# Kernel optimization log

Measured on AMD Instinct MI355X. Metric: run time of the kernel, lower is better.

The kernel has to match this reference:

```python
import jax, jax.numpy as jnp
import numpy as np

IN_MODES = (4, 4, 8, 8, 4)
OUT_MODES = (4, 4, 8, 8, 4)
RANKS = (1, 8, 8, 8, 8, 1)
N_TOKENS = 8192


def setup_inputs() -> dict:
    key = jax.random.key(0)
    ks = jax.random.split(key, 7)
    inp = jax.random.normal(ks[0], (N_TOKENS, int(np.prod(IN_MODES))), dtype=jnp.float32)
    cores = []
    for i in range(5):
        shape = (IN_MODES[i], RANKS[i], RANKS[i + 1], OUT_MODES[i])
        # kaiming-uniform-like small init to keep the 5-core chain numerically tame
        fan_in = shape[0] * shape[1] * shape[2]
        bound = float(np.sqrt(3.0 / fan_in))
        cores.append(jax.random.uniform(ks[i + 1], shape, minval=-bound, maxval=bound, dtype=jnp.float32))
    biases = jax.random.uniform(ks[6], (int(np.prod(OUT_MODES)),), minval=-0.05, maxval=0.05, dtype=jnp.float32)
    return {
        "input": inp,
        "core0": cores[0], "core1": cores[1], "core2": cores[2],
        "core3": cores[3], "core4": cores[4],
        "biases": biases,
    }


def reference(input, core0, core1, core2, core3, core4, biases):
    # reshape tokens into the 5 input modes: [N, a, b, c, d, e]
    x = input.reshape((-1,) + IN_MODES)
    # TT contraction. Original einsum has no '->'; free indices h (ranks[0]=1)
    # and m (ranks[5]=1) are size-1 boundary ranks, so summing them out here is
    # equivalent to the original reshape-squeeze.
    out = jnp.einsum(
        'nabcde,ahiv,bijw,cjkx,dkly,elmz->nvwxyz',
        x, core0, core1, core2, core3, core4,
        optimize='optimal',
    )
    out = out.reshape(-1, int(np.prod(OUT_MODES)))
    return out + biases
```

## Files before the change

kernel.cpp:

```cpp
#include <hip/hip_runtime.h>

#define DIM 4096

typedef __bf16 bf16x8 __attribute__((ext_vector_type(8)));
typedef float floatx4 __attribute__((ext_vector_type(4)));

__device__ __forceinline__ void async_ld16(void* lds, const void* g) {
  __builtin_amdgcn_global_load_lds(
      (const __attribute__((address_space(1))) unsigned int*)g,
      (__attribute__((address_space(3))) unsigned int*)lds, 16, 0, 0);
}

__global__ void build_k(const float* __restrict__ c0, const float* __restrict__ c1,
                        const float* __restrict__ c2, const float* __restrict__ c3,
                        const float* __restrict__ c4,
                        float* __restrict__ K012, float* __restrict__ K34T) {
  const int bid = blockIdx.x, tid = threadIdx.x;
  if (bid < 512) {
    __shared__ float K01s[128];
    const int abc = bid >> 2;
    const int ab = abc >> 3, c = abc & 7;
    if (tid < 128) {
      const int a = ab >> 2, b = ab & 3;
      const int j = tid >> 4, vw = tid & 15, v = vw >> 2, w = vw & 3;
      float s = 0.f;
#pragma unroll
      for (int i = 0; i < 8; ++i)
        s += c0[a * 32 + i * 4 + v] * c1[b * 256 + i * 32 + j * 4 + w];
      K01s[tid] = s;
    }
    __syncthreads();
    const int t = bid * 256 + tid;
    const int vwx = t & 127, k = (t >> 7) & 7;
    const int vw = vwx >> 3, xx = vwx & 7;
    float s = 0.f;
#pragma unroll
    for (int j = 0; j < 8; ++j)
      s += K01s[j * 16 + vw] * c2[c * 512 + j * 64 + k * 8 + xx];
    K012[t] = s;
  } else {
    const int u = (bid - 512) * 256 + tid;
    const int yz = u & 31, kk = (u >> 5) & 7, de = u >> 8;
    const int d = de >> 2, e = de & 3, y = yz >> 2, z = yz & 3;
    float s = 0.f;
#pragma unroll
    for (int l = 0; l < 8; ++l)
      s += c3[d * 512 + kk * 64 + l * 8 + y] * c4[e * 32 + l * 4 + z];
    K34T[kk * 1024 + yz * 32 + de] = s;
  }
}

__global__ void build_wt_conv(const float* __restrict__ K012, const float* __restrict__ K34T,
                              __bf16* __restrict__ WT,
                              const float* __restrict__ X, __bf16* __restrict__ Xb) {
  const int bid = blockIdx.x, tid = threadIdx.x;
  if (bid < 8192) {
    const long t = (long)bid * 256 + tid;
    const long e8 = t * 8;
    const int in = (int)(e8 & 4095), o = (int)(e8 >> 12);
    const int de0 = in & 31, abc = in >> 5;
    const int yz = o & 31, vwx = o >> 5;
    const float* kp = K012 + abc * 1024 + vwx;
    const float* vp = K34T + yz * 32 + de0;
    float s[8] = {};
#pragma unroll
    for (int k = 0; k < 8; ++k) {
      const float a = kp[k * 128];
      const float4 v0 = *(const float4*)(vp + k * 1024);
      const float4 v1 = *(const float4*)(vp + k * 1024 + 4);
      s[0] += a * v0.x; s[1] += a * v0.y; s[2] += a * v0.z; s[3] += a * v0.w;
      s[4] += a * v1.x; s[5] += a * v1.y; s[6] += a * v1.z; s[7] += a * v1.w;
    }
    bf16x8 w;
#pragma unroll
    for (int d = 0; d < 8; ++d) w[d] = (__bf16)s[d];
    ((bf16x8*)WT)[t] = w;
  } else {
    const long t = (long)(bid - 8192) * 256 + tid;
    const float4 a = ((const float4*)X)[t * 2];
    const float4 b = ((const float4*)X)[t * 2 + 1];
    bf16x8 w;
    w[0] = (__bf16)a.x; w[1] = (__bf16)a.y; w[2] = (__bf16)a.z; w[3] = (__bf16)a.w;
    w[4] = (__bf16)b.x; w[5] = (__bf16)b.y; w[6] = (__bf16)b.z; w[7] = (__bf16)b.w;
    ((bf16x8*)Xb)[t] = w;
  }
}


#define SB0()  __builtin_amdgcn_sched_barrier(0)
#define LGKM0() asm volatile("s_waitcnt lgkmcnt(0)" ::: "memory")
#define VM6()  asm volatile("s_waitcnt vmcnt(6)" ::: "memory")
#define BAR()  __builtin_amdgcn_s_barrier()
#define P1() __builtin_amdgcn_s_setprio(1)
#define P0() __builtin_amdgcn_s_setprio(0)

#define STA(p, h, koff) do { \
  async_ld16(&As[p][(h) * 128][0] + ldsq[0], agp[0] + (h) * 524288 + (koff)); \
  async_ld16(&As[p][(h) * 128][0] + ldsq[1], agp[1] + (h) * 524288 + (koff)); } while (0)
#define STB(p, h, koff) do { \
  async_ld16(&Bs[p][(h) * 128][0] + ldsq[0], bgp[0] + (h) * 524288 + (koff)); \
  async_ld16(&Bs[p][(h) * 128][0] + ldsq[1], bgp[1] + (h) * 524288 + (koff)); } while (0)

#define RDA(p, mh) do { \
  _Pragma("unroll") for (int fi = 0; fi < 4; ++fi) { \
    const int row = ((mh) * 8 + 2 * fi + wm) * 16 + lm; \
    _Pragma("unroll") for (int kh = 0; kh < 2; ++kh) \
      af[fi][kh] = *(const bf16x8*)&As[p][row][((kh * 4 + kq) ^ (row & 7)) * 8]; \
  } } while (0)
#define RDB(p, nh, sl) do { \
  _Pragma("unroll") for (int gi = 0; gi < 2; ++gi) { \
    const int row = (4 * ((nh) * 2 + gi) + wn) * 16 + lm; \
    _Pragma("unroll") for (int kh = 0; kh < 2; ++kh) \
      bs[sl][gi][kh] = *(const bf16x8*)&Bs[p][row][((kh * 4 + kq) ^ (row & 7)) * 8]; \
  } } while (0)

#define MMAQ(sl, mh, nh) do { \
  _Pragma("unroll") for (int fi = 0; fi < 4; ++fi) \
  _Pragma("unroll") for (int gi = 0; gi < 2; ++gi) \
  _Pragma("unroll") for (int kh = 0; kh < 2; ++kh) \
    acc[(mh) * 4 + fi][(nh) * 2 + gi] = __builtin_amdgcn_mfma_f32_16x16x32_bf16( \
        af[fi][kh], bs[sl][gi][kh], acc[(mh) * 4 + fi][(nh) * 2 + gi], 0, 0, 0); } while (0)

__global__ __launch_bounds__(512, 2) void gemm_8ph(const __bf16* __restrict__ A,
                                                   const __bf16* __restrict__ WT,
                                                   const float* __restrict__ bias,
                                                   float* __restrict__ C) {
  __shared__ __bf16 As[2][256][64];
  __shared__ __bf16 Bs[2][256][64];

  const int tid = threadIdx.x;
  const int gb = (blockIdx.x & 7) * 64 + (blockIdx.x >> 3);
  const int m0 = (gb >> 4) * 256;
  const int n0 = (gb & 15) * 256;

  const int wave = tid >> 6, lane = tid & 63;
  const int wm = wave & 1, wn = wave >> 1;
  const int lm = lane & 15, kq = lane >> 4;

  floatx4 acc[8][4] = {};
  bf16x8 af[4][2], bs[2][2][2];

  const __bf16* agp[2];
  const __bf16* bgp[2];
  int ldsq[2];
#pragma unroll
  for (int j = 0; j < 2; ++j) {
    const int q = tid + j * 512;
    const int r = q >> 3, pc = q & 7;
    const int c = pc ^ (r & 7);
    ldsq[j] = q * 8;
    agp[j] = A + (long)(m0 + r) * DIM + c * 8;
    bgp[j] = WT + (long)(n0 + r) * DIM + c * 8;
  }

  STB(0, 0, 0); STA(0, 0, 0); STB(0, 1, 0); STA(0, 1, 0); STB(1, 0, 64);
  STA(1, 0, 64); STB(1, 1, 64); STA(1, 1, 64);
  VM6();
  BAR(); SB0();
  RDB(0, 0, 0);

#pragma unroll 1
  for (int it = 0; it < 32; ++it) {
    int t2 = 2 * it + 2; if (t2 > 63) t2 = 63;
    int t3 = 2 * it + 3; if (t3 > 63) t3 = 63;
    const int k2 = t2 * 64, k3 = t3 * 64;

    RDA(0, 0); STB(0, 0, k2);
    BAR(); LGKM0(); SB0(); P1(); MMAQ(0, 0, 0); P0(); BAR(); SB0();

    RDB(0, 1, 1); STA(0, 0, k2);
    BAR(); LGKM0(); SB0(); P1(); MMAQ(1, 0, 1); P0(); BAR(); SB0();

    RDA(0, 1); STB(0, 1, k2);
    BAR(); LGKM0(); SB0(); P1(); MMAQ(1, 1, 1); P0(); BAR(); SB0();

    RDB(1, 0, 1); STA(0, 1, k2);
    BAR(); SB0(); P1(); MMAQ(0, 1, 0); P0();
    LGKM0();
    VM6();
    BAR(); SB0();

    RDA(1, 0); STB(1, 0, k3);
    BAR(); LGKM0(); SB0(); P1(); MMAQ(1, 0, 0); P0(); BAR(); SB0();

    RDB(1, 1, 0); STA(1, 0, k3);
    BAR(); LGKM0(); SB0(); P1(); MMAQ(0, 0, 1); P0(); BAR(); SB0();

    RDA(1, 1); STB(1, 1, k3);
    BAR(); LGKM0(); SB0(); P1(); MMAQ(0, 1, 1); P0(); BAR(); SB0();

    RDB(0, 0, 0); STA(1, 1, k3);
    BAR(); SB0(); P1(); MMAQ(1, 1, 0); P0();
    LGKM0();
    VM6();
    BAR(); SB0();
  }

  float bv[4];
#pragma unroll
  for (int g = 0; g < 4; ++g) bv[g] = bias[n0 + (4 * g + wn) * 16 + lm];
#pragma unroll
  for (int f = 0; f < 8; ++f) {
    const long mr = m0 + (2 * f + wm) * 16 + kq * 4;
#pragma unroll
    for (int g = 0; g < 4; ++g) {
      float* cp = C + mr * DIM + n0 + (4 * g + wn) * 16 + lm;
      cp[0]       = acc[f][g][0] + bv[g];
      cp[DIM]     = acc[f][g][1] + bv[g];
      cp[2 * DIM] = acc[f][g][2] + bv[g];
      cp[3 * DIM] = acc[f][g][3] + bv[g];
    }
  }
}

__global__ __launch_bounds__(256) void gemm_xw(const float* __restrict__ X,
                                               const __bf16* __restrict__ WT,
                                               const float* __restrict__ bias,
                                               float* __restrict__ C) {
  __shared__ __bf16 Asf[128 * 40];
  __shared__ __bf16 Bsf[128 * 32];

  const int tid = threadIdx.x;
  const int n0 = (blockIdx.x & 31) * 128;
  const int m0 = (blockIdx.x >> 5) * 128;

  const int wave = tid >> 6, lane = tid & 63;
  const int wm = (wave >> 1) * 64, wn = (wave & 1) * 64;
  const int lm = lane & 15, kq = lane >> 4;

  floatx4 acc[4][4] = {};

  const int ar = tid >> 1;
  const int ac = (tid & 1) * 16;
  const float* xp = X + (long)(m0 + ar) * DIM + ac;
  __bf16* as_dst = &Asf[ar * 40 + ac];

  const int u0 = tid, u1 = 256 + tid;
  const int r0 = u0 >> 2, r1 = u1 >> 2;
  const int ch0 = (u0 & 3) ^ (r0 & 3), ch1 = (u1 & 3) ^ (r1 & 3);
  const __bf16* wp0 = WT + (long)(n0 + r0) * DIM + ch0 * 8;
  const __bf16* wp1 = WT + (long)(n0 + r1) * DIM + ch1 * 8;

  float4 a0 = *(const float4*)(xp);
  float4 a1 = *(const float4*)(xp + 4);
  float4 a2 = *(const float4*)(xp + 8);
  float4 a3 = *(const float4*)(xp + 12);

#pragma unroll 1
  for (int k0 = 0; k0 < DIM; k0 += 32) {
    async_ld16(&Bsf[u0 * 8], wp0 + k0);
    async_ld16(&Bsf[u1 * 8], wp1 + k0);

    bf16x8 w0, w1;
    w0[0] = (__bf16)a0.x; w0[1] = (__bf16)a0.y; w0[2] = (__bf16)a0.z; w0[3] = (__bf16)a0.w;
    w0[4] = (__bf16)a1.x; w0[5] = (__bf16)a1.y; w0[6] = (__bf16)a1.z; w0[7] = (__bf16)a1.w;
    w1[0] = (__bf16)a2.x; w1[1] = (__bf16)a2.y; w1[2] = (__bf16)a2.z; w1[3] = (__bf16)a2.w;
    w1[4] = (__bf16)a3.x; w1[5] = (__bf16)a3.y; w1[6] = (__bf16)a3.z; w1[7] = (__bf16)a3.w;
    *(bf16x8*)(as_dst) = w0;
    *(bf16x8*)(as_dst + 8) = w1;

    if (k0 + 32 < DIM) {
      a0 = *(const float4*)(xp + k0 + 32);
      a1 = *(const float4*)(xp + k0 + 36);
      a2 = *(const float4*)(xp + k0 + 40);
      a3 = *(const float4*)(xp + k0 + 44);
    }
    __syncthreads();

    bf16x8 afv[4], bfr[4];
#pragma unroll
    for (int mi = 0; mi < 4; ++mi)
      afv[mi] = *(const bf16x8*)&Asf[(wm + mi * 16 + lm) * 40 + kq * 8];
#pragma unroll
    for (int ni = 0; ni < 4; ++ni) {
      int rr = wn + ni * 16 + lm;
      bfr[ni] = *(const bf16x8*)&Bsf[rr * 32 + ((kq ^ (rr & 3)) * 8)];
    }
#pragma unroll
    for (int mi = 0; mi < 4; ++mi)
#pragma unroll
      for (int ni = 0; ni < 4; ++ni)
        acc[mi][ni] = __builtin_amdgcn_mfma_f32_16x16x32_bf16(afv[mi], bfr[ni], acc[mi][ni], 0, 0, 0);
    __syncthreads();
  }

  float bv[4];
#pragma unroll
  for (int ni = 0; ni < 4; ++ni) bv[ni] = bias[n0 + wn + ni * 16 + lm];
#pragma unroll
  for (int mi = 0; mi < 4; ++mi) {
    long mr = m0 + wm + mi * 16 + kq * 4;
#pragma unroll
    for (int ni = 0; ni < 4; ++ni) {
      float* cp = C + mr * DIM + (n0 + wn + ni * 16 + lm);
      cp[0]       = acc[mi][ni][0] + bv[ni];
      cp[DIM]     = acc[mi][ni][1] + bv[ni];
      cp[2 * DIM] = acc[mi][ni][2] + bv[ni];
      cp[3 * DIM] = acc[mi][ni][3] + bv[ni];
    }
  }
}

extern "C" void kernel_launch(void* const* d_in, const int* in_sizes, int n_in,
                              void* d_out, int out_size, void* d_ws, size_t ws_size,
                              hipStream_t stream) {
  const float* x    = (const float*)d_in[0];
  const float* c0   = (const float*)d_in[1];
  const float* c1   = (const float*)d_in[2];
  const float* c2   = (const float*)d_in[3];
  const float* c3   = (const float*)d_in[4];
  const float* c4   = (const float*)d_in[5];
  const float* bias = (const float*)d_in[6];
  float* out = (float*)d_out;

  const size_t XB_SZ = 67108864;
  const size_t WT_SZ = 33554432;
  const size_t K012_SZ = 524288;
  const size_t K34_SZ = 32768;
  char* ws = (char*)d_ws;

  if (ws_size >= XB_SZ + WT_SZ + K012_SZ + K34_SZ) {
    __bf16* Xb  = (__bf16*)ws;
    __bf16* WT  = (__bf16*)(ws + XB_SZ);
    float* K012 = (float*)(ws + XB_SZ + WT_SZ);
    float* K34T = (float*)(ws + XB_SZ + WT_SZ + K012_SZ);

    build_k<<<544, 256, 0, stream>>>(c0, c1, c2, c3, c4, K012, K34T);
    build_wt_conv<<<24576, 256, 0, stream>>>(K012, K34T, WT, x, Xb);
    gemm_8ph<<<512, 512, 0, stream>>>(Xb, WT, bias, out);
  } else {
    __bf16* WT  = (__bf16*)ws;
    float* K012 = (float*)(ws + WT_SZ);
    float* K34T = (float*)(ws + WT_SZ + K012_SZ);

    build_k<<<544, 256, 0, stream>>>(c0, c1, c2, c3, c4, K012, K34T);
    build_wt_conv<<<8192, 256, 0, stream>>>(K012, K34T, WT, x, (__bf16*)nullptr);
    gemm_xw<<<2048, 256, 0, stream>>>(x, WT, bias, out);
  }
}
```

Measured before the change: 491.7 us.

## Restage GEMM pipeline, precompute LDS read addresses, cache K012 in shared memory

The build_wt_conv weight-expansion blocks now load their K012 slice into shared memory once per block instead of issuing strided global loads per thread. In the GEMM, swizzled LDS read addresses are precomputed into per-lane base pointers, which removes per-read index arithmetic. The 8-phase main loop is reordered so A and B fragments for a phase are read together and global-to-LDS stages are shifted one slot, dropping the clamped tail indices. The new order and wait counts risk LDS read/write hazards and may load past K at the last iteration.

```diff
diff --git a/kernel.cpp b/kernel.cpp
--- a/kernel.cpp
+++ b/kernel.cpp
@@ -55,17 +55,25 @@
                               const float* __restrict__ X, __bf16* __restrict__ Xb) {
   const int bid = blockIdx.x, tid = threadIdx.x;
   if (bid < 8192) {
-    const long t = (long)bid * 256 + tid;
-    const long e8 = t * 8;
-    const int in = (int)(e8 & 4095), o = (int)(e8 >> 12);
-    const int de0 = in & 31, abc = in >> 5;
-    const int yz = o & 31, vwx = o >> 5;
-    const float* kp = K012 + abc * 1024 + vwx;
+    __shared__ float Ks[512];
+    const int o = bid >> 1;
+    const int vwx = o >> 5, yz = o & 31;
+    const int abc0 = (bid & 1) * 64;
+#pragma unroll
+    for (int e = tid; e < 512; e += 256)
+      Ks[e] = K012[(abc0 + (e >> 3)) * 1024 + (e & 7) * 128 + vwx];
+    __syncthreads();
+
+    const int in = (bid & 1) * 2048 + tid * 8;
+    const int de0 = in & 31, abcl = (in >> 5) - abc0;
     const float* vp = K34T + yz * 32 + de0;
+    float kk[8];
+#pragma unroll
+    for (int k = 0; k < 8; ++k) kk[k] = Ks[abcl * 8 + k];
     float s[8] = {};
 #pragma unroll
     for (int k = 0; k < 8; ++k) {
-      const float a = kp[k * 128];
+      const float a = kk[k];
       const float4 v0 = *(const float4*)(vp + k * 1024);
       const float4 v1 = *(const float4*)(vp + k * 1024 + 4);
       s[0] += a * v0.x; s[1] += a * v0.y; s[2] += a * v0.z; s[3] += a * v0.w;
@@ -74,7 +82,7 @@
     bf16x8 w;
 #pragma unroll
     for (int d = 0; d < 8; ++d) w[d] = (__bf16)s[d];
-    ((bf16x8*)WT)[t] = w;
+    ((bf16x8*)WT)[(long)bid * 256 + tid] = w;
   } else {
     const long t = (long)(bid - 8192) * 256 + tid;
     const float4 a = ((const float4*)X)[t * 2];
@@ -102,17 +110,15 @@
   async_ld16(&Bs[p][(h) * 128][0] + ldsq[1], bgp[1] + (h) * 524288 + (koff)); } while (0)
 
 #define RDA(p, mh) do { \
-  _Pragma("unroll") for (int fi = 0; fi < 4; ++fi) { \
-    const int row = ((mh) * 8 + 2 * fi + wm) * 16 + lm; \
-    _Pragma("unroll") for (int kh = 0; kh < 2; ++kh) \
-      af[fi][kh] = *(const bf16x8*)&As[p][row][((kh * 4 + kq) ^ (row & 7)) * 8]; \
-  } } while (0)
+  _Pragma("unroll") for (int fi = 0; fi < 4; ++fi) \
+  _Pragma("unroll") for (int kh = 0; kh < 2; ++kh) \
+    af[fi][kh] = *(const bf16x8*)(aB[kh] + (p) * 32768 + ((mh) * 8 + 2 * fi) * 2048); \
+  } while (0)
 #define RDB(p, nh, sl) do { \
-  _Pragma("unroll") for (int gi = 0; gi < 2; ++gi) { \
-    const int row = (4 * ((nh) * 2 + gi) + wn) * 16 + lm; \
-    _Pragma("unroll") for (int kh = 0; kh < 2; ++kh) \
-      bs[sl][gi][kh] = *(const bf16x8*)&Bs[p][row][((kh * 4 + kq) ^ (row & 7)) * 8]; \
-  } } while (0)
+  _Pragma("unroll") for (int gi = 0; gi < 2; ++gi) \
+  _Pragma("unroll") for (int kh = 0; kh < 2; ++kh) \
+    bs[sl][gi][kh] = *(const bf16x8*)(bB[kh] + (p) * 32768 + ((nh) * 2 + gi) * 8192); \
+  } while (0)
 
 #define MMAQ(sl, mh, nh) do { \
   _Pragma("unroll") for (int fi = 0; fi < 4; ++fi) \
@@ -139,6 +145,15 @@
 
   floatx4 acc[8][4] = {};
   bf16x8 af[4][2], bs[2][2][2];
+
+  const char* aB[2];
+  const char* bB[2];
+#pragma unroll
+  for (int k = 0; k < 2; ++k) {
+    const int pcv = ((k * 4 + kq) ^ (lm & 7)) * 16;
+    aB[k] = (const char*)As + (wm * 16 + lm) * 128 + pcv;
+    bB[k] = (const char*)Bs + (wn * 16 + lm) * 128 + pcv;
+  }
 
   const __bf16* agp[2];
   const __bf16* bgp[2];
@@ -153,45 +168,42 @@
     bgp[j] = WT + (long)(n0 + r) * DIM + c * 8;
   }
 
-  STB(0, 0, 0); STA(0, 0, 0); STB(0, 1, 0); STA(0, 1, 0); STB(1, 0, 64);
-  STA(1, 0, 64); STB(1, 1, 64); STA(1, 1, 64);
+  STB(0, 0, 0); STA(0, 0, 0); STB(0, 1, 0); STA(0, 1, 0);
+  STB(1, 0, 64); STA(1, 0, 64); STB(1, 1, 64);
   VM6();
   BAR(); SB0();
-  RDB(0, 0, 0);
 
 #pragma unroll 1
   for (int it = 0; it < 32; ++it) {
-    int t2 = 2 * it + 2; if (t2 > 63) t2 = 63;
-    int t3 = 2 * it + 3; if (t3 > 63) t3 = 63;
-    const int k2 = t2 * 64, k3 = t3 * 64;
-
-    RDA(0, 0); STB(0, 0, k2);
+    const int k1 = (2 * it + 1) * 64;
+    const int k2 = (2 * it + 2) * 64;
+    const int k3 = (2 * it + 3) * 64;
+
+    RDA(0, 0); RDB(0, 0, 0); STA(1, 1, k1);
     BAR(); LGKM0(); SB0(); P1(); MMAQ(0, 0, 0); P0(); BAR(); SB0();
 
-    RDB(0, 1, 1); STA(0, 0, k2);
+    RDB(0, 1, 1); STB(0, 0, k2);
     BAR(); LGKM0(); SB0(); P1(); MMAQ(1, 0, 1); P0(); BAR(); SB0();
 
-    RDA(0, 1); STB(0, 1, k2);
+    RDA(0, 1); STA(0, 0, k2);
     BAR(); LGKM0(); SB0(); P1(); MMAQ(1, 1, 1); P0(); BAR(); SB0();
 
-    RDB(1, 0, 1); STA(0, 1, k2);
+    STB(0, 1, k2);
     BAR(); SB0(); P1(); MMAQ(0, 1, 0); P0();
-    LGKM0();
     VM6();
     BAR(); SB0();
 
-    RDA(1, 0); STB(1, 0, k3);
-    BAR(); LGKM0(); SB0(); P1(); MMAQ(1, 0, 0); P0(); BAR(); SB0();
-
-    RDB(1, 1, 0); STA(1, 0, k3);
-    BAR(); LGKM0(); SB0(); P1(); MMAQ(0, 0, 1); P0(); BAR(); SB0();
-
-    RDA(1, 1); STB(1, 1, k3);
-    BAR(); LGKM0(); SB0(); P1(); MMAQ(0, 1, 1); P0(); BAR(); SB0();
-
-    RDB(0, 0, 0); STA(1, 1, k3);
-    BAR(); SB0(); P1(); MMAQ(1, 1, 0); P0();
-    LGKM0();
+    RDA(1, 0); RDB(1, 0, 0); STA(0, 1, k2);
+    BAR(); LGKM0(); SB0(); P1(); MMAQ(0, 0, 0); P0(); BAR(); SB0();
+
+    RDB(1, 1, 1); STB(1, 0, k3);
+    BAR(); LGKM0(); SB0(); P1(); MMAQ(1, 0, 1); P0(); BAR(); SB0();
+
+    RDA(1, 1); STA(1, 0, k3);
+    BAR(); LGKM0(); SB0(); P1(); MMAQ(1, 1, 1); P0(); BAR(); SB0();
+
+    STB(1, 1, k3);
+    BAR(); SB0(); P1(); MMAQ(0, 1, 0); P0();
     VM6();
     BAR(); SB0();
   }
```

Measured after the change: 486.0 us. No clear change (-1.2%).
